# Kernel optimization log

Hardware: AMD Instinct MI355X
Metric: run time of the kernel (lower is better)

The kernel has to match this reference:

```python
import jax, jax.numpy as jnp
import numpy as np

EPS = 1e-06

def phi(x):
    # canonical linear-attention feature map: elu(x) + 1 (positive features)
    return jax.nn.elu(x) + 1.0

def setup_inputs() -> dict:
    key = jax.random.key(0)
    kq, kk, kv = jax.random.split(key, 3)
    B, H, S, D = 4, 16, 4096, 64
    query = jax.random.normal(kq, (B, H, S, D), dtype=jnp.float32)
    k = jax.random.normal(kk, (B, H, S, D), dtype=jnp.float32)
    value = jax.random.normal(kv, (B, H, S, D), dtype=jnp.float32)
    attention_mask = jnp.ones((B, S), dtype=jnp.float32)
    return {"query": query, "key": k, "value": value, "attention_mask": attention_mask}

def reference(query, key, value, attention_mask):
    B, H, S, D = query.shape
    q = query / jnp.sqrt(jnp.asarray(D, query.dtype))
    phi_q = phi(q)                                   # [b,h,n,d]
    phi_k = phi(key)                                 # [b,h,n,d]
    mask = attention_mask[:, None, :, None].astype(phi_k.dtype)  # [b,1,n,1]
    phi_k = phi_k * mask
    kv_term = jnp.einsum('bhnd,bhnv->bhdv', phi_k, value)        # [b,h,d,v]
    output = jnp.einsum('bhnd,bhdv->bhnv', phi_q, kv_term)       # [b,h,n,v]
    k_one = jnp.sum(phi_k, axis=2)                               # [b,h,d] == phi_k @ masked ones
    normalizer = jnp.einsum('bhnd,bhd->bhn', phi_q, k_one)[..., None]  # [b,h,n,1]
    return output / (normalizer + EPS)
```

## Files before the change

kernel.cpp:

```cpp
#include <hip/hip_runtime.h>

typedef unsigned short ushort_t;
typedef unsigned int uint32;
typedef __bf16 bf16x8 __attribute__((ext_vector_type(8)));
typedef float f32x4 __attribute__((ext_vector_type(4)));

#define NB 4
#define NH 16
#define NS 4096
#define ND 64
#define NBH 64
#define EPSF 1e-6f

#define CH1 16
#define ROWS1 (NS / CH1)
#define P2R 64
#define LDJ 70
#define LDJW 35
#define BTSZ (80 * 64)

__device__ __forceinline__ float phi_f(float x) {
    return x > 0.0f ? x + 1.0f : __expf(x);
}
__device__ __forceinline__ ushort_t bf16_rn(float x) {
    uint32 u = __float_as_uint(x);
    uint32 r = (u + 0x7FFFu + ((u >> 16) & 1u)) >> 16;
    return (ushort_t)r;
}
__device__ __forceinline__ void split2(float x, ushort_t& h, ushort_t& l) {
    h = bf16_rn(x);
    float hf = __uint_as_float(((uint32)h) << 16);
    l = bf16_rn(x - hf);
}
union FragU { uint32 u[4]; bf16x8 v; };
__device__ __forceinline__ bf16x8 ld_frag(const ushort_t* arr, int widx) {
    const uint32* p = (const uint32*)arr;
    FragU f;
    f.u[0] = p[widx]; f.u[1] = p[widx + 1]; f.u[2] = p[widx + 2]; f.u[3] = p[widx + 3];
    return f.v;
}
union FragP { ushort_t s[8]; bf16x8 v; };
__device__ __forceinline__ bf16x8 ld_frag16(const ushort_t* arr, int off16) {
    return *(const bf16x8*)(arr + off16);
}
__device__ __forceinline__ f32x4 mfma16(bf16x8 a, bf16x8 b, f32x4 c) {
    return __builtin_amdgcn_mfma_f32_16x16x32_bf16(a, b, c, 0, 0, 0);
}

template<bool PART>
__global__ __launch_bounds__(256, 4)
void la_pass1(const float* __restrict__ Kin, const float* __restrict__ Vin,
              const float* __restrict__ Min, float* __restrict__ okv,
              float* __restrict__ ok1)
{
    const int t  = threadIdx.x;
    const int cx = blockIdx.x;
    const int bh = blockIdx.y;
    const int bb = bh >> 4;
    const float* Kb = Kin + (long long)bh * NS * ND;
    const float* Vb = Vin + (long long)bh * NS * ND;
    const float* Mb = Min + (long long)bb * NS;

    __shared__ __align__(16) ushort_t skh[64 * LDJ], skl[64 * LDJ];
    __shared__ __align__(16) ushort_t svh[64 * LDJ], svl[64 * LDJ];

    const int rr0 = t >> 4;
    const int c   = (t & 15) * 4;
    const int wv  = t >> 6;
    const int m   = t & 15;
    const int q   = (t & 63) >> 4;

    const f32x4 zf = {0.f, 0.f, 0.f, 0.f};
    f32x4 acc0 = zf, acc1 = zf, acc2 = zf, acc3 = zf;
    float k1loc[4] = {0.f, 0.f, 0.f, 0.f};

    const int s0 = cx * ROWS1;

    float4 k4[4], v4[4];
    float  mk[4];
#define LOADT(tt) { \
        const long long rb_ = (long long)(s0 + (tt) * 64 + rr0); \
        const float* kp_ = Kb + rb_ * ND + c; \
        const float* vp_ = Vb + rb_ * ND + c; \
        k4[0] = *(const float4*)(kp_);            v4[0] = *(const float4*)(vp_); \
        k4[1] = *(const float4*)(kp_ + 16 * ND);  v4[1] = *(const float4*)(vp_ + 16 * ND); \
        k4[2] = *(const float4*)(kp_ + 32 * ND);  v4[2] = *(const float4*)(vp_ + 32 * ND); \
        k4[3] = *(const float4*)(kp_ + 48 * ND);  v4[3] = *(const float4*)(vp_ + 48 * ND); \
        mk[0] = Mb[rb_]; mk[1] = Mb[rb_ + 16]; mk[2] = Mb[rb_ + 32]; mk[3] = Mb[rb_ + 48]; }

    LOADT(0);

    for (int tile = 0; tile < ROWS1 / 64; ++tile) {
        __syncthreads();
        #pragma unroll
        for (int j = 0; j < 4; ++j) {
            const int rr = rr0 + 16 * j;
            const float xs[4] = {k4[j].x, k4[j].y, k4[j].z, k4[j].w};
            const float vs[4] = {v4[j].x, v4[j].y, v4[j].z, v4[j].w};
            #pragma unroll
            for (int i = 0; i < 4; ++i) {
                const float x = phi_f(xs[i]) * mk[j];
                k1loc[i] += x;
                ushort_t h, l;
                split2(x, h, l);
                skh[(c + i) * LDJ + rr] = h;
                skl[(c + i) * LDJ + rr] = l;
                split2(vs[i], h, l);
                svh[(c + i) * LDJ + rr] = h;
                svl[(c + i) * LDJ + rr] = l;
            }
        }
        if (tile + 1 < ROWS1 / 64) LOADT(tile + 1);
        __syncthreads();
        #pragma unroll
        for (int ks = 0; ks < 2; ++ks) {
            const int fo = ks * 16 + q * 4;
            const bf16x8 ah = ld_frag(skh, (16 * wv + m) * LDJW + fo);
            const bf16x8 al = ld_frag(skl, (16 * wv + m) * LDJW + fo);
            {
                const bf16x8 fbh = ld_frag(svh, (0 + m) * LDJW + fo);
                const bf16x8 fbl = ld_frag(svl, (0 + m) * LDJW + fo);
                acc0 = mfma16(al, fbh, acc0); acc0 = mfma16(ah, fbl, acc0); acc0 = mfma16(ah, fbh, acc0);
            }
            {
                const bf16x8 fbh = ld_frag(svh, (16 + m) * LDJW + fo);
                const bf16x8 fbl = ld_frag(svl, (16 + m) * LDJW + fo);
                acc1 = mfma16(al, fbh, acc1); acc1 = mfma16(ah, fbl, acc1); acc1 = mfma16(ah, fbh, acc1);
            }
            {
                const bf16x8 fbh = ld_frag(svh, (32 + m) * LDJW + fo);
                const bf16x8 fbl = ld_frag(svl, (32 + m) * LDJW + fo);
                acc2 = mfma16(al, fbh, acc2); acc2 = mfma16(ah, fbl, acc2); acc2 = mfma16(ah, fbh, acc2);
            }
            {
                const bf16x8 fbh = ld_frag(svh, (48 + m) * LDJW + fo);
                const bf16x8 fbl = ld_frag(svl, (48 + m) * LDJW + fo);
                acc3 = mfma16(al, fbh, acc3); acc3 = mfma16(ah, fbl, acc3); acc3 = mfma16(ah, fbh, acc3);
            }
        }
    }
#undef LOADT

    const int dbase = 16 * wv + q * 4;
    if (PART) {
        float* outp = okv + (long long)(bh * CH1 + cx) * (ND * ND);
        #pragma unroll
        for (int i = 0; i < 4; ++i) {
            outp[(dbase + i) * ND +  0 + m] = acc0[i];
            outp[(dbase + i) * ND + 16 + m] = acc1[i];
            outp[(dbase + i) * ND + 32 + m] = acc2[i];
            outp[(dbase + i) * ND + 48 + m] = acc3[i];
        }
    } else {
        float* outp = okv + (long long)bh * (ND * ND);
        #pragma unroll
        for (int i = 0; i < 4; ++i) {
            atomicAdd(&outp[(dbase + i) * ND +  0 + m], acc0[i]);
            atomicAdd(&outp[(dbase + i) * ND + 16 + m], acc1[i]);
            atomicAdd(&outp[(dbase + i) * ND + 32 + m], acc2[i]);
            atomicAdd(&outp[(dbase + i) * ND + 48 + m], acc3[i]);
        }
    }
    __syncthreads();
    float* red = (float*)skh;
    #pragma unroll
    for (int i = 0; i < 4; ++i) red[(c + i) * 17 + rr0] = k1loc[i];
    __syncthreads();
    if (t < 64) {
        float s = 0.f;
        #pragma unroll
        for (int g = 0; g < 16; ++g) s += red[t * 17 + g];
        if (PART) ok1[(bh * CH1 + cx) * ND + t] = s;
        else      atomicAdd(&ok1[bh * ND + t], s);
    }
}

__global__ __launch_bounds__(256)
void la_reduce(const float* __restrict__ pkv, const float* __restrict__ pk1,
               ushort_t* __restrict__ BTh, ushort_t* __restrict__ BTl)
{
    const int t = threadIdx.x;
    const int bh = blockIdx.x;
    const float4* src = (const float4*)(pkv + (long long)bh * CH1 * ND * ND);
    float4 a[4];
    #pragma unroll
    for (int i = 0; i < 4; ++i) { a[i].x = 0.f; a[i].y = 0.f; a[i].z = 0.f; a[i].w = 0.f; }
    for (int c = 0; c < CH1; ++c) {
        #pragma unroll
        for (int i = 0; i < 4; ++i) {
            const float4 v = src[c * 1024 + t + 256 * i];
            a[i].x += v.x; a[i].y += v.y; a[i].z += v.z; a[i].w += v.w;
        }
    }
    ushort_t* oh = BTh + (long long)bh * BTSZ;
    ushort_t* ol = BTl + (long long)bh * BTSZ;
    #pragma unroll
    for (int i = 0; i < 4; ++i) {
        const int e4 = t + 256 * i;
        const int d  = e4 >> 4;
        const int v0 = (e4 & 15) * 4;
        const float vals[4] = {a[i].x, a[i].y, a[i].z, a[i].w};
        #pragma unroll
        for (int j = 0; j < 4; ++j) {
            ushort_t h, l; split2(vals[j], h, l);
            oh[(v0 + j) * ND + d] = h;
            ol[(v0 + j) * ND + d] = l;
        }
    }
    if (t < ND) {
        float s = 0.f;
        for (int c = 0; c < CH1; ++c) s += pk1[(bh * CH1 + c) * ND + t];
        ushort_t h, l; split2(s, h, l);
        oh[64 * ND + t] = h; ol[64 * ND + t] = l;
    }
    for (int z = t; z < 15 * 64; z += 256) { oh[65 * ND + z] = 0; ol[65 * ND + z] = 0; }
}

__global__ __launch_bounds__(256)
void la_convert(const float* __restrict__ kv, const float* __restrict__ k1,
                ushort_t* __restrict__ BTh, ushort_t* __restrict__ BTl)
{
    const int t = threadIdx.x;
    const int bh = blockIdx.x;
    const float* kvb = kv + (long long)bh * ND * ND;
    ushort_t* oh = BTh + (long long)bh * BTSZ;
    ushort_t* ol = BTl + (long long)bh * BTSZ;
    for (int e = t; e < ND * ND; e += 256) {
        const int d = e >> 6, v = e & 63;
        ushort_t h, l; split2(kvb[e], h, l);
        oh[v * ND + d] = h; ol[v * ND + d] = l;
    }
    if (t < ND) { ushort_t h, l; split2(k1[bh * ND + t], h, l); oh[64 * ND + t] = h; ol[64 * ND + t] = l; }
    for (int z = t; z < 15 * 64; z += 256) { oh[65 * ND + z] = 0; ol[65 * ND + z] = 0; }
}

__global__ __launch_bounds__(256, 6)
void la_pass2(const float* __restrict__ Qin, const ushort_t* __restrict__ BTh,
              const ushort_t* __restrict__ BTl, float* __restrict__ Out)
{
    const int t  = threadIdx.x;
    const int bh = blockIdx.y;
    const int s0 = blockIdx.x * P2R;
    const long long base = (long long)bh * NS * ND;
    const int wv = t >> 6;
    const int m  = t & 15;
    const int q  = (t & 63) >> 4;
    const int lane = t & 63;
    const ushort_t* Bh = BTh + (long long)bh * BTSZ;
    const ushort_t* Bl = BTl + (long long)bh * BTSZ;

    bf16x8 aH[2], aL[2];
    {
        const int row = s0 + 16 * wv + m;
        const float* qp = Qin + base + (long long)row * ND;
        float4 x0[2], x1[2];
        #pragma unroll
        for (int ks = 0; ks < 2; ++ks) {
            x0[ks] = *(const float4*)(qp + ks * 32 + q * 8);
            x1[ks] = *(const float4*)(qp + ks * 32 + q * 8 + 4);
        }
        #pragma unroll
        for (int ks = 0; ks < 2; ++ks) {
            const float xs[8] = {x0[ks].x, x0[ks].y, x0[ks].z, x0[ks].w,
                                 x1[ks].x, x1[ks].y, x1[ks].z, x1[ks].w};
            FragP fh, fl;
            #pragma unroll
            for (int i = 0; i < 8; ++i) {
                ushort_t h, l; split2(phi_f(xs[i] * 0.125f), h, l);
                fh.s[i] = h; fl.s[i] = l;
            }
            aH[ks] = fh.v; aL[ks] = fl.v;
        }
    }

    const f32x4 zf = {0.f, 0.f, 0.f, 0.f};
    f32x4 acc[5];
    #pragma unroll
    for (int b = 0; b < 5; ++b) acc[b] = zf;

    #pragma unroll
    for (int nt = 0; nt < 5; ++nt) {
        #pragma unroll
        for (int ks = 0; ks < 2; ++ks) {
            const int bo = (16 * nt + m) * ND + ks * 32 + q * 8;
            const bf16x8 fbh = ld_frag16(Bh, bo);
            const bf16x8 fbl = ld_frag16(Bl, bo);
            acc[nt] = mfma16(aL[ks], fbh, acc[nt]);
            acc[nt] = mfma16(aH[ks], fbl, acc[nt]);
            acc[nt] = mfma16(aH[ks], fbh, acc[nt]);
        }
    }

    float* outb = Out + base;
    const int rbase = s0 + 16 * wv + q * 4;
    #pragma unroll
    for (int i = 0; i < 4; ++i) {
        const float nv = __shfl(acc[4][i], lane & 48, 64);
        const float rn = 1.0f / (nv + EPSF);
        const long long ro = (long long)(rbase + i) * ND;
        outb[ro +  0 + m] = acc[0][i] * rn;
        outb[ro + 16 + m] = acc[1][i] * rn;
        outb[ro + 32 + m] = acc[2][i] * rn;
        outb[ro + 48 + m] = acc[3][i] * rn;
    }
}

extern "C" void kernel_launch(void* const* d_in, const int* in_sizes, int n_in,
                              void* d_out, int out_size, void* d_ws, size_t ws_size,
                              hipStream_t stream)
{
    const float* Q = (const float*)d_in[0];
    const float* K = (const float*)d_in[1];
    const float* V = (const float*)d_in[2];
    const float* M = (const float*)d_in[3];
    float* Out = (float*)d_out;

    const size_t partf = (size_t)NBH * CH1 * ND * ND;
    const size_t pk1f  = (size_t)NBH * CH1 * ND;
    const size_t kvf   = (size_t)NBH * ND * ND;
    const size_t k1f   = (size_t)NBH * ND;
    const size_t btu   = (size_t)NBH * BTSZ;
    const size_t need  = (partf + pk1f) * sizeof(float) + 2 * btu * sizeof(ushort_t);

    if (ws_size >= need) {
        float* PKV = (float*)d_ws;
        float* PK1 = PKV + partf;
        ushort_t* BThp = (ushort_t*)(PK1 + pk1f);
        ushort_t* BTlp = BThp + btu;
        la_pass1<true><<<dim3(CH1, NBH), dim3(256), 0, stream>>>(K, V, M, PKV, PK1);
        la_reduce<<<dim3(NBH), dim3(256), 0, stream>>>(PKV, PK1, BThp, BTlp);
        la_pass2<<<dim3(NS / P2R, NBH), dim3(256), 0, stream>>>(Q, BThp, BTlp, Out);
    } else {
        float* KVb = (float*)d_ws;
        float* K1b = KVb + kvf;
        ushort_t* BThp = (ushort_t*)(K1b + k1f);
        ushort_t* BTlp = BThp + btu;
        hipMemsetAsync(d_ws, 0, (kvf + k1f) * sizeof(float), stream);
        la_pass1<false><<<dim3(CH1, NBH), dim3(256), 0, stream>>>(K, V, M, KVb, K1b);
        la_convert<<<dim3(NBH), dim3(256), 0, stream>>>(KVb, K1b, BThp, BTlp);
        la_pass2<<<dim3(NS / P2R, NBH), dim3(256), 0, stream>>>(Q, BThp, BTlp, Out);
    }
}
```

Before: 257.3 us.

## Double-buffer K/V register prefetch and hoist all global loads in pass2

In pass1 the K/V/mask tile loads now go into a two-slot register buffer, and the next tile's load is issued before the current tile is converted. Scheduling barriers keep the compiler from sinking those loads, so global latency overlaps the shared-memory stores and MFMA work. In pass2 the Q loads and all B-fragment loads are issued up front behind a schedule barrier, and launch bounds are relaxed from 6 to 2 blocks per CU. This raises memory-level parallelism at the cost of higher register pressure and possibly lower occupancy.

```diff
diff --git a/kernel.cpp b/kernel.cpp
--- a/kernel.cpp
+++ b/kernel.cpp
@@ -40,9 +40,6 @@
     return f.v;
 }
 union FragP { ushort_t s[8]; bf16x8 v; };
-__device__ __forceinline__ bf16x8 ld_frag16(const ushort_t* arr, int off16) {
-    return *(const bf16x8*)(arr + off16);
-}
 __device__ __forceinline__ f32x4 mfma16(bf16x8 a, bf16x8 b, f32x4 c) {
     return __builtin_amdgcn_mfma_f32_16x16x32_bf16(a, b, c, 0, 0, 0);
 }
@@ -76,30 +73,40 @@
 
     const int s0 = cx * ROWS1;
 
-    float4 k4[4], v4[4];
-    float  mk[4];
-#define LOADT(tt) { \
+    float4 kR[2][4], vR[2][4];
+    float  mR[2][4];
+#define LOADT(tt, sset) { \
         const long long rb_ = (long long)(s0 + (tt) * 64 + rr0); \
         const float* kp_ = Kb + rb_ * ND + c; \
         const float* vp_ = Vb + rb_ * ND + c; \
-        k4[0] = *(const float4*)(kp_);            v4[0] = *(const float4*)(vp_); \
-        k4[1] = *(const float4*)(kp_ + 16 * ND);  v4[1] = *(const float4*)(vp_ + 16 * ND); \
-        k4[2] = *(const float4*)(kp_ + 32 * ND);  v4[2] = *(const float4*)(vp_ + 32 * ND); \
-        k4[3] = *(const float4*)(kp_ + 48 * ND);  v4[3] = *(const float4*)(vp_ + 48 * ND); \
-        mk[0] = Mb[rb_]; mk[1] = Mb[rb_ + 16]; mk[2] = Mb[rb_ + 32]; mk[3] = Mb[rb_ + 48]; }
-
-    LOADT(0);
-
+        kR[sset][0] = *(const float4*)(kp_);            vR[sset][0] = *(const float4*)(vp_); \
+        kR[sset][1] = *(const float4*)(kp_ + 16 * ND);  vR[sset][1] = *(const float4*)(vp_ + 16 * ND); \
+        kR[sset][2] = *(const float4*)(kp_ + 32 * ND);  vR[sset][2] = *(const float4*)(vp_ + 32 * ND); \
+        kR[sset][3] = *(const float4*)(kp_ + 48 * ND);  vR[sset][3] = *(const float4*)(vp_ + 48 * ND); \
+        mR[sset][0] = Mb[rb_];      mR[sset][1] = Mb[rb_ + 16]; \
+        mR[sset][2] = Mb[rb_ + 32]; mR[sset][3] = Mb[rb_ + 48]; }
+
+    LOADT(0, 0);
+    __builtin_amdgcn_sched_barrier(0);
+
+    #pragma unroll
     for (int tile = 0; tile < ROWS1 / 64; ++tile) {
+        const int cur = tile & 1;
+        const int nxt = cur ^ 1;
+        if (tile + 1 < ROWS1 / 64) {
+            LOADT(tile + 1, nxt);
+            __builtin_amdgcn_sched_barrier(0);
+        }
         __syncthreads();
         #pragma unroll
         for (int j = 0; j < 4; ++j) {
             const int rr = rr0 + 16 * j;
-            const float xs[4] = {k4[j].x, k4[j].y, k4[j].z, k4[j].w};
-            const float vs[4] = {v4[j].x, v4[j].y, v4[j].z, v4[j].w};
+            const float xs[4] = {kR[cur][j].x, kR[cur][j].y, kR[cur][j].z, kR[cur][j].w};
+            const float vs[4] = {vR[cur][j].x, vR[cur][j].y, vR[cur][j].z, vR[cur][j].w};
+            const float mj = mR[cur][j];
             #pragma unroll
             for (int i = 0; i < 4; ++i) {
-                const float x = phi_f(xs[i]) * mk[j];
+                const float x = phi_f(xs[i]) * mj;
                 k1loc[i] += x;
                 ushort_t h, l;
                 split2(x, h, l);
@@ -110,7 +117,6 @@
                 svl[(c + i) * LDJ + rr] = l;
             }
         }
-        if (tile + 1 < ROWS1 / 64) LOADT(tile + 1);
         __syncthreads();
         #pragma unroll
         for (int ks = 0; ks < 2; ++ks) {
@@ -234,7 +240,7 @@
     for (int z = t; z < 15 * 64; z += 256) { oh[65 * ND + z] = 0; ol[65 * ND + z] = 0; }
 }
 
-__global__ __launch_bounds__(256, 6)
+__global__ __launch_bounds__(256, 2)
 void la_pass2(const float* __restrict__ Qin, const ushort_t* __restrict__ BTh,
               const ushort_t* __restrict__ BTl, float* __restrict__ Out)
 {
@@ -249,28 +255,37 @@
     const ushort_t* Bh = BTh + (long long)bh * BTSZ;
     const ushort_t* Bl = BTl + (long long)bh * BTSZ;
 
+    const int row = s0 + 16 * wv + m;
+    const float* qp = Qin + base + (long long)row * ND;
+    float4 qv[4];
+    qv[0] = *(const float4*)(qp + q * 8);
+    qv[1] = *(const float4*)(qp + q * 8 + 4);
+    qv[2] = *(const float4*)(qp + 32 + q * 8);
+    qv[3] = *(const float4*)(qp + 32 + q * 8 + 4);
+    bf16x8 fbh[5][2], fbl[5][2];
+    #pragma unroll
+    for (int nt = 0; nt < 5; ++nt) {
+        #pragma unroll
+        for (int ks = 0; ks < 2; ++ks) {
+            const int bo = (16 * nt + m) * ND + ks * 32 + q * 8;
+            fbh[nt][ks] = *(const bf16x8*)(Bh + bo);
+            fbl[nt][ks] = *(const bf16x8*)(Bl + bo);
+        }
+    }
+    __builtin_amdgcn_sched_barrier(0);
+
     bf16x8 aH[2], aL[2];
-    {
-        const int row = s0 + 16 * wv + m;
-        const float* qp = Qin + base + (long long)row * ND;
-        float4 x0[2], x1[2];
-        #pragma unroll
-        for (int ks = 0; ks < 2; ++ks) {
-            x0[ks] = *(const float4*)(qp + ks * 32 + q * 8);
-            x1[ks] = *(const float4*)(qp + ks * 32 + q * 8 + 4);
-        }
-        #pragma unroll
-        for (int ks = 0; ks < 2; ++ks) {
-            const float xs[8] = {x0[ks].x, x0[ks].y, x0[ks].z, x0[ks].w,
-                                 x1[ks].x, x1[ks].y, x1[ks].z, x1[ks].w};
-            FragP fh, fl;
-            #pragma unroll
-            for (int i = 0; i < 8; ++i) {
-                ushort_t h, l; split2(phi_f(xs[i] * 0.125f), h, l);
-                fh.s[i] = h; fl.s[i] = l;
-            }
-            aH[ks] = fh.v; aL[ks] = fl.v;
-        }
+    #pragma unroll
+    for (int ks = 0; ks < 2; ++ks) {
+        const float xs[8] = {qv[2 * ks].x, qv[2 * ks].y, qv[2 * ks].z, qv[2 * ks].w,
+                             qv[2 * ks + 1].x, qv[2 * ks + 1].y, qv[2 * ks + 1].z, qv[2 * ks + 1].w};
+        FragP fh, fl;
+        #pragma unroll
+        for (int i = 0; i < 8; ++i) {
+            ushort_t h, l; split2(phi_f(xs[i] * 0.125f), h, l);
+            fh.s[i] = h; fl.s[i] = l;
+        }
+        aH[ks] = fh.v; aL[ks] = fl.v;
     }
 
     const f32x4 zf = {0.f, 0.f, 0.f, 0.f};
@@ -282,12 +297,9 @@
     for (int nt = 0; nt < 5; ++nt) {
         #pragma unroll
         for (int ks = 0; ks < 2; ++ks) {
-            const int bo = (16 * nt + m) * ND + ks * 32 + q * 8;
-            const bf16x8 fbh = ld_frag16(Bh, bo);
-            const bf16x8 fbl = ld_frag16(Bl, bo);
-            acc[nt] = mfma16(aL[ks], fbh, acc[nt]);
-            acc[nt] = mfma16(aH[ks], fbl, acc[nt]);
-            acc[nt] = mfma16(aH[ks], fbh, acc[nt]);
+            acc[nt] = mfma16(aL[ks], fbh[nt][ks], acc[nt]);
+            acc[nt] = mfma16(aH[ks], fbl[nt][ks], acc[nt]);
+            acc[nt] = mfma16(aH[ks], fbh[nt][ks], acc[nt]);
         }
     }
 
```

Result: slower. 272.6 us (+6.0%).
